# Kernel optimization log

Hardware: AMD Instinct MI355X
Metric: run time of the kernel (lower is better)

## Reference

```python
import jax, jax.numpy as jnp
import numpy as np

N_NODES = 1_000_000
N_EDGES = 20_000_000


def setup_inputs() -> dict:
    key = jax.random.key(0)
    k_row, k_col, k_attr = jax.random.split(key, 3)
    # Guarantee every row appears at least once so row-sums are > 0
    # (the original module implicitly assumes no zero-degree rows).
    row_tail = jax.random.randint(k_row, (N_EDGES - N_NODES,), 0, N_NODES, dtype=jnp.int32)
    row = jnp.concatenate([jnp.arange(N_NODES, dtype=jnp.int32), row_tail])
    col = jax.random.randint(k_col, (N_EDGES,), 0, N_NODES, dtype=jnp.int32)
    edge_index = jnp.stack([row, col])  # [2, E]
    # Positive edge weights keep the reciprocal well-conditioned.
    edge_attr = jax.random.uniform(k_attr, (N_EDGES,), dtype=jnp.float32,
                                   minval=0.1, maxval=1.0)
    return {"edge_index": edge_index, "edge_attr": edge_attr, "N": N_NODES}


def reference(edge_index, edge_attr, N):
    # spmm(edge_index, edge_attr, N, N, ones) == per-row sum of edge weights
    rowsum = jax.ops.segment_sum(edge_attr, edge_index[0], num_segments=N)  # [N]
    rownorm = 1.0 / rowsum                                                  # [N]
    # Gather normalization factor at the COLUMN index of each edge, then scale.
    return rownorm[edge_index[1]] * edge_attr                                # [E]
```

## Files before the change

kernel.cpp:

```cpp
#include <hip/hip_runtime.h>
#include <hip/hip_fp16.h>
#include <stdint.h>


typedef int      v4i __attribute__((ext_vector_type(4)));
typedef float    v4f __attribute__((ext_vector_type(4)));
typedef unsigned v4u __attribute__((ext_vector_type(4)));
using ull = unsigned long long;

#define BKT_BITS 13
#define BKT_W    (1 << BKT_BITS)
#define NB       128
#define NMAX     (NB << BKT_BITS)
#define TILE     4096
#define BLOCK1   512
#define BLOCK2   1024


__global__ __launch_bounds__(BLOCK1) void hist_kernel(
    const int* __restrict__ row, int* __restrict__ histG, int E)
{
    __shared__ int h[NB];
    const int t = threadIdx.x;
    const long base = (long)blockIdx.x * TILE;
    if (t < NB) h[t] = 0;
    __syncthreads();
    if (base + TILE <= (long)E) {
        #pragma unroll
        for (int k = 0; k < 2; ++k) {
            const long e0 = base + ((long)(k * BLOCK1 + t) << 2);
            const v4i rv = __builtin_nontemporal_load(reinterpret_cast<const v4i*>(row + e0));
            atomicAdd(&h[rv.x >> BKT_BITS], 1);
            atomicAdd(&h[rv.y >> BKT_BITS], 1);
            atomicAdd(&h[rv.z >> BKT_BITS], 1);
            atomicAdd(&h[rv.w >> BKT_BITS], 1);
        }
    } else {
        for (int k = 0; k < 2; ++k) {
            const long e0 = base + ((long)(k * BLOCK1 + t) << 2);
            for (int j = 0; j < 4; ++j)
                if (e0 + j < (long)E) atomicAdd(&h[row[e0 + j] >> BKT_BITS], 1);
        }
    }
    __syncthreads();
    if (t < NB) histG[(size_t)blockIdx.x * NB + t] = h[t];
}

__global__ __launch_bounds__(256) void totals_kernel(
    const int* __restrict__ histG, int* __restrict__ totals, int nTiles)
{
    __shared__ int s[256];
    const int b = blockIdx.x;
    int acc = 0;
    for (int t = threadIdx.x; t < nTiles; t += 256)
        acc += histG[(size_t)t * NB + b];
    s[threadIdx.x] = acc;
    __syncthreads();
    for (int o = 128; o > 0; o >>= 1) {
        if (threadIdx.x < o) s[threadIdx.x] += s[threadIdx.x + o];
        __syncthreads();
    }
    if (threadIdx.x == 0) totals[b] = s[0];
}

__global__ __launch_bounds__(NB) void bases_kernel(
    const int* __restrict__ totals, int* __restrict__ bases)
{
    __shared__ int s[NB];
    const int t = threadIdx.x;
    const int rc = (totals[t] + 1) & ~1;
    s[t] = rc;
    __syncthreads();
    for (int off = 1; off < NB; off <<= 1) {
        const int v = (t >= off) ? s[t - off] : 0;
        __syncthreads();
        s[t] += v;
        __syncthreads();
    }
    bases[t] = s[t] - rc;
}

__global__ __launch_bounds__(256) void offsets_kernel(
    const int* __restrict__ histG, const int* __restrict__ bases,
    int* __restrict__ offG, int nTiles)
{
    __shared__ int s[256];
    const int b = blockIdx.x;
    const int seg = (nTiles + 255) >> 8;
    const int t0 = threadIdx.x * seg;
    int acc = 0;
    for (int k = 0; k < seg; ++k) {
        const int t = t0 + k;
        if (t < nTiles) acc += histG[(size_t)t * NB + b];
    }
    s[threadIdx.x] = acc;
    __syncthreads();
    for (int off = 1; off < 256; off <<= 1) {
        const int v = (threadIdx.x >= off) ? s[threadIdx.x - off] : 0;
        __syncthreads();
        s[threadIdx.x] += v;
        __syncthreads();
    }
    int run = bases[b] + s[threadIdx.x] - acc;
    for (int k = 0; k < seg; ++k) {
        const int t = t0 + k;
        if (t < nTiles) {
            offG[(size_t)t * NB + b] = run;
            run += histG[(size_t)t * NB + b];
        }
    }
}

__global__ __launch_bounds__(BLOCK1) void scatter_kernel(
    const int* __restrict__ row, const float* __restrict__ attr,
    const int* __restrict__ offG, ull* __restrict__ pairsG, int E)
{
    __shared__ int cnt[NB];
    __shared__ int scanb[NB];
    __shared__ int gbase[NB];
    __shared__ ull pairs[TILE];

    const int  t    = threadIdx.x;
    const long base = (long)blockIdx.x * TILE;
    const bool full = (base + TILE <= (long)E);

    if (t < NB) cnt[t] = 0;
    __syncthreads();

    int r[8]; float a[8]; int rk[8];
    if (full) {
        #pragma unroll
        for (int k = 0; k < 2; ++k) {
            const long e0 = base + ((long)(k * BLOCK1 + t) << 2);
            const v4i rv = __builtin_nontemporal_load(reinterpret_cast<const v4i*>(row + e0));
            const v4f av = __builtin_nontemporal_load(reinterpret_cast<const v4f*>(attr + e0));
            r[k*4+0]=rv.x; r[k*4+1]=rv.y; r[k*4+2]=rv.z; r[k*4+3]=rv.w;
            a[k*4+0]=av.x; a[k*4+1]=av.y; a[k*4+2]=av.z; a[k*4+3]=av.w;
        }
        #pragma unroll
        for (int i = 0; i < 8; ++i)
            rk[i] = atomicAdd(&cnt[r[i] >> BKT_BITS], 1);
    } else {
        for (int k = 0; k < 2; ++k) {
            const long e0 = base + ((long)(k * BLOCK1 + t) << 2);
            for (int j = 0; j < 4; ++j) {
                const int i = k*4 + j;
                if (e0 + j < (long)E) {
                    r[i] = row[e0 + j]; a[i] = attr[e0 + j];
                    rk[i] = atomicAdd(&cnt[r[i] >> BKT_BITS], 1);
                } else r[i] = -1;
            }
        }
    }
    __syncthreads();

    if (t < 64) {
        const int h0 = cnt[2*t], h1 = cnt[2*t+1];
        const int sum = h0 + h1;
        int x = sum;
        #pragma unroll
        for (int off = 1; off < 64; off <<= 1) {
            const int y = __shfl_up(x, off);
            if (t >= off) x += y;
        }
        const int excl = x - sum;
        scanb[2*t]   = excl;
        scanb[2*t+1] = excl + h0;
    }
    if (t < NB) gbase[t] = offG[(size_t)blockIdx.x * NB + t];
    __syncthreads();

    #pragma unroll
    for (int i = 0; i < 8; ++i)
        if (r[i] >= 0)
            pairs[scanb[r[i] >> BKT_BITS] + rk[i]] =
                ((ull)__float_as_uint(a[i]) << 32) | (unsigned)r[i];
    __syncthreads();

    const int total = full ? TILE : (int)((long)E - base);
    for (int s = t; s < total; s += BLOCK1) {
        const ull p  = pairs[s];
        const int bb = (int)(((unsigned)p) >> BKT_BITS);
        const size_t dst = (size_t)gbase[bb] + (size_t)(s - scanb[bb]);
        __builtin_nontemporal_store(p, pairsG + dst);
    }
}

__global__ __launch_bounds__(BLOCK2) void reduce_kernel(
    const ull* __restrict__ pairsG, const int* __restrict__ totals,
    const int* __restrict__ bases, float* __restrict__ partial, int nSplit)
{
    __shared__ float bins[BKT_W];
    const int b = blockIdx.x / nSplit;
    const int q = blockIdx.x % nSplit;
    for (int i = threadIdx.x; i < BKT_W; i += BLOCK2) bins[i] = 0.0f;
    __syncthreads();

    const int cnt = totals[b];
    const ull* src = pairsG + (size_t)bases[b];
    const int Q = cnt >> 2;
    for (int i = q * BLOCK2 + threadIdx.x; i < Q; i += nSplit * BLOCK2) {
        const v4u p0 = __builtin_nontemporal_load(reinterpret_cast<const v4u*>(src + 4*(size_t)i));
        const v4u p1 = __builtin_nontemporal_load(reinterpret_cast<const v4u*>(src + 4*(size_t)i + 2));
        atomicAdd(&bins[p0.x & (BKT_W-1)], __uint_as_float(p0.y));
        atomicAdd(&bins[p0.z & (BKT_W-1)], __uint_as_float(p0.w));
        atomicAdd(&bins[p1.x & (BKT_W-1)], __uint_as_float(p1.y));
        atomicAdd(&bins[p1.z & (BKT_W-1)], __uint_as_float(p1.w));
    }
    const int rem = cnt - (Q << 2);
    if (q == 0 && threadIdx.x < rem) {
        const ull p = src[(Q << 2) + threadIdx.x];
        atomicAdd(&bins[(unsigned)p & (BKT_W-1)], __uint_as_float((unsigned)(p >> 32)));
    }
    __syncthreads();

    float* dst = partial + (size_t)q * NMAX + ((size_t)b << BKT_BITS);
    for (int i = threadIdx.x; i < BKT_W; i += BLOCK2)
        __builtin_nontemporal_store(bins[i], dst + i);
}

__global__ void recip_kernel(const float* __restrict__ partial,
                             __half* __restrict__ rnorm16,
                             const int* __restrict__ Np, int nSplit) {
    const int N = *Np;
    const int stride = gridDim.x * blockDim.x;
    for (int i = blockIdx.x * blockDim.x + threadIdx.x; i < N; i += stride) {
        float s = 0.0f;
        for (int q = 0; q < nSplit; ++q) s += partial[(size_t)q * NMAX + i];
        rnorm16[i] = __float2half(1.0f / s);
    }
}


__global__ __launch_bounds__(256) void gather_scale_f16_kernel(
    const int* __restrict__ col, const float* __restrict__ attr,
    const __half* __restrict__ rn, float* __restrict__ out, int E)
{
    const int tid = blockIdx.x * blockDim.x + threadIdx.x;
    const int stride = gridDim.x * blockDim.x;
    const int E4 = E >> 2;
    const v4i* col4  = reinterpret_cast<const v4i*>(col);
    const v4f* attr4 = reinterpret_cast<const v4f*>(attr);
    v4f*       out4  = reinterpret_cast<v4f*>(out);

    int i = tid;
    for (; i + 3 * stride < E4; i += 4 * stride) {
        const v4i c0 = __builtin_nontemporal_load(col4 + i);
        const v4i c1 = __builtin_nontemporal_load(col4 + i + stride);
        const v4i c2 = __builtin_nontemporal_load(col4 + i + 2 * stride);
        const v4i c3 = __builtin_nontemporal_load(col4 + i + 3 * stride);
        const v4f a0 = __builtin_nontemporal_load(attr4 + i);
        const v4f a1 = __builtin_nontemporal_load(attr4 + i + stride);
        const v4f a2 = __builtin_nontemporal_load(attr4 + i + 2 * stride);
        const v4f a3 = __builtin_nontemporal_load(attr4 + i + 3 * stride);
        v4f o0, o1, o2, o3;
        o0.x = __half2float(rn[c0.x]) * a0.x; o0.y = __half2float(rn[c0.y]) * a0.y;
        o0.z = __half2float(rn[c0.z]) * a0.z; o0.w = __half2float(rn[c0.w]) * a0.w;
        o1.x = __half2float(rn[c1.x]) * a1.x; o1.y = __half2float(rn[c1.y]) * a1.y;
        o1.z = __half2float(rn[c1.z]) * a1.z; o1.w = __half2float(rn[c1.w]) * a1.w;
        o2.x = __half2float(rn[c2.x]) * a2.x; o2.y = __half2float(rn[c2.y]) * a2.y;
        o2.z = __half2float(rn[c2.z]) * a2.z; o2.w = __half2float(rn[c2.w]) * a2.w;
        o3.x = __half2float(rn[c3.x]) * a3.x; o3.y = __half2float(rn[c3.y]) * a3.y;
        o3.z = __half2float(rn[c3.z]) * a3.z; o3.w = __half2float(rn[c3.w]) * a3.w;
        __builtin_nontemporal_store(o0, out4 + i);
        __builtin_nontemporal_store(o1, out4 + i + stride);
        __builtin_nontemporal_store(o2, out4 + i + 2 * stride);
        __builtin_nontemporal_store(o3, out4 + i + 3 * stride);
    }
    for (; i < E4; i += stride) {
        const v4i c = __builtin_nontemporal_load(col4 + i);
        const v4f a = __builtin_nontemporal_load(attr4 + i);
        v4f o;
        o.x = __half2float(rn[c.x]) * a.x; o.y = __half2float(rn[c.y]) * a.y;
        o.z = __half2float(rn[c.z]) * a.z; o.w = __half2float(rn[c.w]) * a.w;
        __builtin_nontemporal_store(o, out4 + i);
    }
    for (int e = (E4 << 2) + tid; e < E; e += stride)
        out[e] = __half2float(rn[col[e]]) * attr[e];
}


__global__ void zero_ws_kernel(float* __restrict__ ws, const int* __restrict__ Np) {
    const int N = *Np;
    const int stride = gridDim.x * blockDim.x;
    for (int i = blockIdx.x * blockDim.x + threadIdx.x; i < N; i += stride)
        ws[i] = 0.0f;
}

__global__ void rowsum_atomic_kernel(const int* __restrict__ row,
                                     const float* __restrict__ attr,
                                     float* __restrict__ rowsum, int E) {
    const int tid = blockIdx.x * blockDim.x + threadIdx.x;
    const int stride = gridDim.x * blockDim.x;
    const int E4 = E >> 2;
    for (int i = tid; i < E4; i += stride) {
        const int4   r = reinterpret_cast<const int4*>(row)[i];
        const float4 a = reinterpret_cast<const float4*>(attr)[i];
        atomicAdd(&rowsum[r.x], a.x);
        atomicAdd(&rowsum[r.y], a.y);
        atomicAdd(&rowsum[r.z], a.z);
        atomicAdd(&rowsum[r.w], a.w);
    }
    for (int i = (E4 << 2) + tid; i < E; i += stride)
        atomicAdd(&rowsum[row[i]], attr[i]);
}

__global__ void recip_fallback_kernel(float* __restrict__ rowsum,
                                      const int* __restrict__ Np) {
    const int N = *Np;
    const int stride = gridDim.x * blockDim.x;
    for (int i = blockIdx.x * blockDim.x + threadIdx.x; i < N; i += stride)
        rowsum[i] = 1.0f / rowsum[i];
}

__global__ __launch_bounds__(256) void gather_scale_f32_kernel(
    const int* __restrict__ col, const float* __restrict__ attr,
    const float* __restrict__ rnorm, float* __restrict__ out, int E)
{
    const int tid = blockIdx.x * blockDim.x + threadIdx.x;
    const int stride = gridDim.x * blockDim.x;
    const int E4 = E >> 2;
    const v4i* col4  = reinterpret_cast<const v4i*>(col);
    const v4f* attr4 = reinterpret_cast<const v4f*>(attr);
    v4f*       out4  = reinterpret_cast<v4f*>(out);
    for (int i = tid; i < E4; i += stride) {
        const v4i c = __builtin_nontemporal_load(col4 + i);
        const v4f a = __builtin_nontemporal_load(attr4 + i);
        v4f o;
        o.x = rnorm[c.x] * a.x; o.y = rnorm[c.y] * a.y;
        o.z = rnorm[c.z] * a.z; o.w = rnorm[c.w] * a.w;
        __builtin_nontemporal_store(o, out4 + i);
    }
    for (int e = (E4 << 2) + tid; e < E; e += stride)
        out[e] = rnorm[col[e]] * attr[e];
}


extern "C" void kernel_launch(void* const* d_in, const int* in_sizes, int n_in,
                              void* d_out, int out_size, void* d_ws, size_t ws_size,
                              hipStream_t stream) {
    const int*   edge_index = (const int*)d_in[0];
    const float* edge_attr  = (const float*)d_in[1];
    const int*   Np         = (const int*)d_in[2];

    const int E = in_sizes[1];
    const int* row = edge_index;
    const int* col = edge_index + E;
    float* out = (float*)d_out;

    const int nTiles = (E + TILE - 1) / TILE;
    auto align256 = [](size_t x) { return (x + 255) & ~(size_t)255; };

    size_t off = 0;
    const size_t basesOff  = off; off += align256(NB * sizeof(int));
    const size_t totalsOff = off; off += align256(NB * sizeof(int));
    const size_t rn16Off   = off; off += align256((size_t)NMAX * sizeof(__half));
    const size_t partOff   = off;
    const size_t histBytes = align256((size_t)nTiles * NB * sizeof(int));
    const size_t scanBytes = 2 * histBytes;
    const size_t pairsBytes = ((size_t)E + 2 * NB) * sizeof(ull);

    int nSplit = 0;
    size_t partRegion = 0;
    for (int c : {8, 4, 2, 1}) {
        size_t pr = (size_t)c * NMAX * sizeof(float);
        if (pr < scanBytes) pr = scanBytes;
        if (partOff + pr + pairsBytes <= ws_size) { nSplit = c; partRegion = pr; break; }
    }

    if (nSplit > 0) {
        int*    bases   = (int*)   ((char*)d_ws + basesOff);
        int*    totals  = (int*)   ((char*)d_ws + totalsOff);
        __half* rnorm16 = (__half*)((char*)d_ws + rn16Off);
        float*  partial = (float*) ((char*)d_ws + partOff);
        int*    histG   = (int*)   ((char*)d_ws + partOff);
        int*    offG    = (int*)   ((char*)d_ws + partOff + histBytes);
        ull*    pairs   = (ull*)   ((char*)d_ws + partOff + partRegion);

        hist_kernel           <<<nTiles, BLOCK1, 0, stream>>>(row, histG, E);
        totals_kernel         <<<NB, 256, 0, stream>>>(histG, totals, nTiles);
        bases_kernel          <<<1, NB, 0, stream>>>(totals, bases);
        offsets_kernel        <<<NB, 256, 0, stream>>>(histG, bases, offG, nTiles);
        scatter_kernel        <<<nTiles, BLOCK1, 0, stream>>>(row, edge_attr, offG, pairs, E);
        reduce_kernel         <<<NB * nSplit, BLOCK2, 0, stream>>>(pairs, totals, bases, partial, nSplit);
        recip_kernel          <<<1024, 256, 0, stream>>>(partial, rnorm16, Np, nSplit);
        gather_scale_f16_kernel<<<2048, 256, 0, stream>>>(col, edge_attr, rnorm16, out, E);
    } else {
        float* rowsum = (float*)d_ws;
        const int workE = (E + 3) >> 2;
        int gE = (workE + 255) / 256;
        if (gE > 2048) gE = 2048;
        zero_ws_kernel        <<<2048, 256, 0, stream>>>(rowsum, Np);
        rowsum_atomic_kernel  <<<gE, 256, 0, stream>>>(row, edge_attr, rowsum, E);
        recip_fallback_kernel <<<2048, 256, 0, stream>>>(rowsum, Np);
        gather_scale_f32_kernel<<<2048, 256, 0, stream>>>(col, edge_attr, rowsum, out, E);
    }
}
```

Measured before the change: 398.2 us.

## Split bucket pairs into separate float values and 16-bit ids; one-shot gather grid

Scatter now writes edge weights and 13-bit in-bucket row ids to two separate arrays (float plus u16) instead of packed 64-bit pairs. The intermediate shrinks from 8 to 6 bytes per edge, cutting write and read traffic in the scatter and reduce kernels. The reduce kernel reads 8 ids and 8 values per thread, and bucket bases are aligned to 8 so those vector loads stay aligned. Separately, the gather kernel changes from a grid-stride loop over 2048 blocks to one block per 1024 quads, each thread handling 4 vectors, which means many more small blocks.

New measurement: 462.4 us (median of 2 runs). 16.1% more time.

```diff
diff --git a/kernel.cpp b/kernel.cpp
--- a/kernel.cpp
+++ b/kernel.cpp
@@ -7,6 +7,7 @@
 typedef float    v4f __attribute__((ext_vector_type(4)));
 typedef unsigned v4u __attribute__((ext_vector_type(4)));
 using ull = unsigned long long;
+using u16 = unsigned short;
 
 #define BKT_BITS 13
 #define BKT_W    (1 << BKT_BITS)
@@ -68,7 +69,7 @@
 {
     __shared__ int s[NB];
     const int t = threadIdx.x;
-    const int rc = (totals[t] + 1) & ~1;
+    const int rc = (totals[t] + 7) & ~7;
     s[t] = rc;
     __syncthreads();
     for (int off = 1; off < NB; off <<= 1) {
@@ -113,12 +114,14 @@
 
 __global__ __launch_bounds__(BLOCK1) void scatter_kernel(
     const int* __restrict__ row, const float* __restrict__ attr,
-    const int* __restrict__ offG, ull* __restrict__ pairsG, int E)
-{
-    __shared__ int cnt[NB];
-    __shared__ int scanb[NB];
-    __shared__ int gbase[NB];
-    __shared__ ull pairs[TILE];
+    const int* __restrict__ offG, float* __restrict__ valsG,
+    u16* __restrict__ idsG, int E)
+{
+    __shared__ int   cnt[NB];
+    __shared__ int   scanb[NB];
+    __shared__ int   gbase[NB];
+    __shared__ float pv[TILE];
+    __shared__ int   pr[TILE];
 
     const int  t    = threadIdx.x;
     const long base = (long)blockIdx.x * TILE;
@@ -171,24 +174,29 @@
     __syncthreads();
 
     #pragma unroll
-    for (int i = 0; i < 8; ++i)
-        if (r[i] >= 0)
-            pairs[scanb[r[i] >> BKT_BITS] + rk[i]] =
-                ((ull)__float_as_uint(a[i]) << 32) | (unsigned)r[i];
+    for (int i = 0; i < 8; ++i) {
+        if (r[i] >= 0) {
+            const int pos = scanb[r[i] >> BKT_BITS] + rk[i];
+            pv[pos] = a[i];
+            pr[pos] = r[i];
+        }
+    }
     __syncthreads();
 
     const int total = full ? TILE : (int)((long)E - base);
     for (int s = t; s < total; s += BLOCK1) {
-        const ull p  = pairs[s];
-        const int bb = (int)(((unsigned)p) >> BKT_BITS);
+        const int rr = pr[s];
+        const int bb = rr >> BKT_BITS;
         const size_t dst = (size_t)gbase[bb] + (size_t)(s - scanb[bb]);
-        __builtin_nontemporal_store(p, pairsG + dst);
+        __builtin_nontemporal_store(pv[s], valsG + dst);
+        __builtin_nontemporal_store((u16)(rr & (BKT_W - 1)), idsG + dst);
     }
 }
 
 __global__ __launch_bounds__(BLOCK2) void reduce_kernel(
-    const ull* __restrict__ pairsG, const int* __restrict__ totals,
-    const int* __restrict__ bases, float* __restrict__ partial, int nSplit)
+    const float* __restrict__ valsG, const u16* __restrict__ idsG,
+    const int* __restrict__ totals, const int* __restrict__ bases,
+    float* __restrict__ partial, int nSplit)
 {
     __shared__ float bins[BKT_W];
     const int b = blockIdx.x / nSplit;
@@ -197,20 +205,27 @@
     __syncthreads();
 
     const int cnt = totals[b];
-    const ull* src = pairsG + (size_t)bases[b];
-    const int Q = cnt >> 2;
-    for (int i = q * BLOCK2 + threadIdx.x; i < Q; i += nSplit * BLOCK2) {
-        const v4u p0 = __builtin_nontemporal_load(reinterpret_cast<const v4u*>(src + 4*(size_t)i));
-        const v4u p1 = __builtin_nontemporal_load(reinterpret_cast<const v4u*>(src + 4*(size_t)i + 2));
-        atomicAdd(&bins[p0.x & (BKT_W-1)], __uint_as_float(p0.y));
-        atomicAdd(&bins[p0.z & (BKT_W-1)], __uint_as_float(p0.w));
-        atomicAdd(&bins[p1.x & (BKT_W-1)], __uint_as_float(p1.y));
-        atomicAdd(&bins[p1.z & (BKT_W-1)], __uint_as_float(p1.w));
-    }
-    const int rem = cnt - (Q << 2);
+    const float* srcV = valsG + (size_t)bases[b];
+    const u16*   srcI = idsG  + (size_t)bases[b];
+    const int Q8 = cnt >> 3;
+    for (int i = q * BLOCK2 + threadIdx.x; i < Q8; i += nSplit * BLOCK2) {
+        const size_t o = (size_t)i << 3;
+        const v4u iv = __builtin_nontemporal_load(reinterpret_cast<const v4u*>(srcI + o));
+        const v4f v0 = __builtin_nontemporal_load(reinterpret_cast<const v4f*>(srcV + o));
+        const v4f v1 = __builtin_nontemporal_load(reinterpret_cast<const v4f*>(srcV + o + 4));
+        atomicAdd(&bins[iv.x & 0xFFFF], v0.x);
+        atomicAdd(&bins[iv.x >> 16],    v0.y);
+        atomicAdd(&bins[iv.y & 0xFFFF], v0.z);
+        atomicAdd(&bins[iv.y >> 16],    v0.w);
+        atomicAdd(&bins[iv.z & 0xFFFF], v1.x);
+        atomicAdd(&bins[iv.z >> 16],    v1.y);
+        atomicAdd(&bins[iv.w & 0xFFFF], v1.z);
+        atomicAdd(&bins[iv.w >> 16],    v1.w);
+    }
+    const int rem = cnt - (Q8 << 3);
     if (q == 0 && threadIdx.x < rem) {
-        const ull p = src[(Q << 2) + threadIdx.x];
-        atomicAdd(&bins[(unsigned)p & (BKT_W-1)], __uint_as_float((unsigned)(p >> 32)));
+        const int o = (Q8 << 3) + threadIdx.x;
+        atomicAdd(&bins[srcI[o]], srcV[o]);
     }
     __syncthreads();
 
@@ -232,51 +247,53 @@
 }
 
 
-__global__ __launch_bounds__(256) void gather_scale_f16_kernel(
+__global__ __launch_bounds__(256) void gather_oneshot_kernel(
     const int* __restrict__ col, const float* __restrict__ attr,
     const __half* __restrict__ rn, float* __restrict__ out, int E)
 {
-    const int tid = blockIdx.x * blockDim.x + threadIdx.x;
-    const int stride = gridDim.x * blockDim.x;
     const int E4 = E >> 2;
+    const int t  = threadIdx.x;
     const v4i* col4  = reinterpret_cast<const v4i*>(col);
     const v4f* attr4 = reinterpret_cast<const v4f*>(attr);
     v4f*       out4  = reinterpret_cast<v4f*>(out);
 
-    int i = tid;
-    for (; i + 3 * stride < E4; i += 4 * stride) {
-        const v4i c0 = __builtin_nontemporal_load(col4 + i);
-        const v4i c1 = __builtin_nontemporal_load(col4 + i + stride);
-        const v4i c2 = __builtin_nontemporal_load(col4 + i + 2 * stride);
-        const v4i c3 = __builtin_nontemporal_load(col4 + i + 3 * stride);
-        const v4f a0 = __builtin_nontemporal_load(attr4 + i);
-        const v4f a1 = __builtin_nontemporal_load(attr4 + i + stride);
-        const v4f a2 = __builtin_nontemporal_load(attr4 + i + 2 * stride);
-        const v4f a3 = __builtin_nontemporal_load(attr4 + i + 3 * stride);
-        v4f o0, o1, o2, o3;
-        o0.x = __half2float(rn[c0.x]) * a0.x; o0.y = __half2float(rn[c0.y]) * a0.y;
-        o0.z = __half2float(rn[c0.z]) * a0.z; o0.w = __half2float(rn[c0.w]) * a0.w;
-        o1.x = __half2float(rn[c1.x]) * a1.x; o1.y = __half2float(rn[c1.y]) * a1.y;
-        o1.z = __half2float(rn[c1.z]) * a1.z; o1.w = __half2float(rn[c1.w]) * a1.w;
-        o2.x = __half2float(rn[c2.x]) * a2.x; o2.y = __half2float(rn[c2.y]) * a2.y;
-        o2.z = __half2float(rn[c2.z]) * a2.z; o2.w = __half2float(rn[c2.w]) * a2.w;
-        o3.x = __half2float(rn[c3.x]) * a3.x; o3.y = __half2float(rn[c3.y]) * a3.y;
-        o3.z = __half2float(rn[c3.z]) * a3.z; o3.w = __half2float(rn[c3.w]) * a3.w;
-        __builtin_nontemporal_store(o0, out4 + i);
-        __builtin_nontemporal_store(o1, out4 + i + stride);
-        __builtin_nontemporal_store(o2, out4 + i + 2 * stride);
-        __builtin_nontemporal_store(o3, out4 + i + 3 * stride);
-    }
-    for (; i < E4; i += stride) {
-        const v4i c = __builtin_nontemporal_load(col4 + i);
-        const v4f a = __builtin_nontemporal_load(attr4 + i);
-        v4f o;
-        o.x = __half2float(rn[c.x]) * a.x; o.y = __half2float(rn[c.y]) * a.y;
-        o.z = __half2float(rn[c.z]) * a.z; o.w = __half2float(rn[c.w]) * a.w;
-        __builtin_nontemporal_store(o, out4 + i);
-    }
-    for (int e = (E4 << 2) + tid; e < E; e += stride)
+    const int b0 = blockIdx.x * (256 * 4) + t;
+    int idx[4]; bool ok[4];
+    v4i c[4]; v4f a[4];
+    #pragma unroll
+    for (int k = 0; k < 4; ++k) {
+        idx[k] = b0 + k * 256;
+        ok[k]  = idx[k] < E4;
+    }
+    #pragma unroll
+    for (int k = 0; k < 4; ++k)
+        if (ok[k]) c[k] = __builtin_nontemporal_load(col4 + idx[k]);
+    #pragma unroll
+    for (int k = 0; k < 4; ++k)
+        if (ok[k]) a[k] = __builtin_nontemporal_load(attr4 + idx[k]);
+    float r[4][4];
+    #pragma unroll
+    for (int k = 0; k < 4; ++k) {
+        if (ok[k]) {
+            r[k][0] = __half2float(rn[c[k].x]);
+            r[k][1] = __half2float(rn[c[k].y]);
+            r[k][2] = __half2float(rn[c[k].z]);
+            r[k][3] = __half2float(rn[c[k].w]);
+        }
+    }
+    #pragma unroll
+    for (int k = 0; k < 4; ++k) {
+        if (ok[k]) {
+            v4f o;
+            o.x = r[k][0] * a[k].x; o.y = r[k][1] * a[k].y;
+            o.z = r[k][2] * a[k].z; o.w = r[k][3] * a[k].w;
+            __builtin_nontemporal_store(o, out4 + idx[k]);
+        }
+    }
+    if (blockIdx.x == 0 && t < (E & 3)) {
+        const int e = (E4 << 2) + t;
         out[e] = __half2float(rn[col[e]]) * attr[e];
+    }
 }
 
 
@@ -358,14 +375,16 @@
     const size_t partOff   = off;
     const size_t histBytes = align256((size_t)nTiles * NB * sizeof(int));
     const size_t scanBytes = 2 * histBytes;
-    const size_t pairsBytes = ((size_t)E + 2 * NB) * sizeof(ull);
+    const size_t capE      = (size_t)E + 8 * NB;
+    const size_t valsBytes = align256(capE * sizeof(float));
+    const size_t idsBytes  = align256(capE * sizeof(u16));
 
     int nSplit = 0;
     size_t partRegion = 0;
     for (int c : {8, 4, 2, 1}) {
         size_t pr = (size_t)c * NMAX * sizeof(float);
         if (pr < scanBytes) pr = scanBytes;
-        if (partOff + pr + pairsBytes <= ws_size) { nSplit = c; partRegion = pr; break; }
+        if (partOff + pr + valsBytes + idsBytes <= ws_size) { nSplit = c; partRegion = pr; break; }
     }
 
     if (nSplit > 0) {
@@ -375,16 +394,20 @@
         float*  partial = (float*) ((char*)d_ws + partOff);
         int*    histG   = (int*)   ((char*)d_ws + partOff);
         int*    offG    = (int*)   ((char*)d_ws + partOff + histBytes);
-        ull*    pairs   = (ull*)   ((char*)d_ws + partOff + partRegion);
-
-        hist_kernel           <<<nTiles, BLOCK1, 0, stream>>>(row, histG, E);
-        totals_kernel         <<<NB, 256, 0, stream>>>(histG, totals, nTiles);
-        bases_kernel          <<<1, NB, 0, stream>>>(totals, bases);
-        offsets_kernel        <<<NB, 256, 0, stream>>>(histG, bases, offG, nTiles);
-        scatter_kernel        <<<nTiles, BLOCK1, 0, stream>>>(row, edge_attr, offG, pairs, E);
-        reduce_kernel         <<<NB * nSplit, BLOCK2, 0, stream>>>(pairs, totals, bases, partial, nSplit);
-        recip_kernel          <<<1024, 256, 0, stream>>>(partial, rnorm16, Np, nSplit);
-        gather_scale_f16_kernel<<<2048, 256, 0, stream>>>(col, edge_attr, rnorm16, out, E);
+        float*  valsG   = (float*) ((char*)d_ws + partOff + partRegion);
+        u16*    idsG    = (u16*)   ((char*)d_ws + partOff + partRegion + valsBytes);
+
+        const int E4 = E >> 2;
+        const int gGather = (E4 + 1023) / 1024;
+
+        hist_kernel         <<<nTiles, BLOCK1, 0, stream>>>(row, histG, E);
+        totals_kernel       <<<NB, 256, 0, stream>>>(histG, totals, nTiles);
+        bases_kernel        <<<1, NB, 0, stream>>>(totals, bases);
+        offsets_kernel      <<<NB, 256, 0, stream>>>(histG, bases, offG, nTiles);
+        scatter_kernel      <<<nTiles, BLOCK1, 0, stream>>>(row, edge_attr, offG, valsG, idsG, E);
+        reduce_kernel       <<<NB * nSplit, BLOCK2, 0, stream>>>(valsG, idsG, totals, bases, partial, nSplit);
+        recip_kernel        <<<1024, 256, 0, stream>>>(partial, rnorm16, Np, nSplit);
+        gather_oneshot_kernel<<<gGather, 256, 0, stream>>>(col, edge_attr, rnorm16, out, E);
     } else {
         float* rowsum = (float*)d_ws;
         const int workE = (E + 3) >> 2;
```
